# Kernel optimization log

Measured on AMD Instinct MI355X. Metric: run time of the kernel, lower is better.

Reference implementation:

```python
import jax, jax.numpy as jnp
import numpy as np

V, C, T, H, HS, HID, L = 8000, 256, 256, 4, 64, 1024, 2
B = 2


def _ln(x, g, b, eps=1e-5):
    mu = jnp.mean(x, axis=-1, keepdims=True)
    var = jnp.var(x, axis=-1, keepdims=True)
    return (x - mu) * jax.lax.rsqrt(var + eps) * g + b


def setup_inputs() -> dict:
    key = jax.random.key(0)
    ks = iter(jax.random.split(key, 32))
    n = lambda shape: jax.random.normal(next(ks), shape, dtype=jnp.float32) * 0.02
    inp = {
        "idx": jax.random.randint(next(ks), (B, T), 0, V),
        "tok_emb": n((V, C)),
        # distance positional embedding params
        "pos_table": n((T, C)),
        "pos_w1": n((C, 2 * C)),
        "pos_w2": n((2 * C, 2 * C)),
        "pos_b2": n((2 * C,)),
        "pos_ln_g": jnp.ones((2 * C,), jnp.float32),
        "pos_ln_b": jnp.zeros((2 * C,), jnp.float32),
        # per-layer, per-head attention-MLP params (stacked over L, H)
        "att_w1": n((L, H, 2 * C, C)),
        "att_w2": n((L, H, C)),
        "att_b2": n((L, H)),
        "val_w": n((L, H, C, HS)),
        "proj_w": n((L, C, C)),
        "proj_b": n((L, C)),
        "ln2_g": jnp.ones((L, C), jnp.float32),
        "ln2_b": jnp.zeros((L, C), jnp.float32),
        "ff_w1": n((L, C, HID)),
        "ff_w2": n((L, HID, C)),
        "ff_b2": n((L, C)),
        "lnf_g": jnp.ones((C,), jnp.float32),
        "lnf_b": jnp.zeros((C,), jnp.float32),
        "head_w": n((C, V)),
        "head_b": n((V,)),
    }
    return inp


def reference(idx, tok_emb, pos_table, pos_w1, pos_w2, pos_b2, pos_ln_g, pos_ln_b,
              att_w1, att_w2, att_b2, val_w, proj_w, proj_b, ln2_g, ln2_b,
              ff_w1, ff_w2, ff_b2, lnf_g, lnf_b, head_w, head_b):
    b, t = idx.shape
    gelu = lambda x: jax.nn.gelu(x, approximate=False)

    # distance positional embedding: tril(i - j) indices into table
    ar = jnp.arange(t)
    dist = jnp.tril(ar[:, None] - ar[None, :])            # [t,t] in [0, t)
    pe = pos_table[dist]                                   # [t,t,C]
    pe = gelu(pe @ pos_w1) @ pos_w2 + pos_b2               # [t,t,2C]
    pe = _ln(pe, pos_ln_g, pos_ln_b)                       # [t,t,2C]

    mask = jnp.tril(jnp.ones((t, t), bool))                # causal
    scale = C ** (-0.5)

    x = tok_emb[idx]                                       # [b,t,C]
    for l in range(L):
        # pairwise concat(key, query) + pos emb, shared across heads
        kk = jnp.broadcast_to(x[:, None, :, :], (b, t, t, C))   # k[b,i,j]=x[b,j]
        qq = jnp.broadcast_to(x[:, :, None, :], (b, t, t, C))   # q[b,i,j]=x[b,i]
        a2 = jnp.concatenate([kk, qq], axis=-1) + pe[None]       # [b,t,t,2C]
        h1 = gelu(jnp.einsum('btsz,hzc->bhtsc', a2, att_w1[l]))  # [b,H,t,t,C]
        wei = jnp.einsum('bhtsc,hc->bhts', h1, att_w2[l]) + att_b2[l][None, :, None, None]
        wei = wei * scale
        wei = jnp.where(mask[None, None], wei, -jnp.inf)
        wei = jax.nn.softmax(wei, axis=-1)                       # [b,H,t,t]
        v = jnp.einsum('btc,hcd->bhtd', x, val_w[l])             # [b,H,t,HS]
        out = jnp.einsum('bhts,bhsd->bhtd', wei, v)              # [b,H,t,HS]
        out = out.transpose(0, 2, 1, 3).reshape(b, t, H * HS)    # concat heads
        x = x + out @ proj_w[l] + proj_b[l]
        h = _ln(x, ln2_g[l], ln2_b[l])
        x = x + gelu(h @ ff_w1[l]) @ ff_w2[l] + ff_b2[l]
    x = _ln(x, lnf_g, lnf_b)
    logits = x @ head_w + head_b                                 # [b,t,V]
    return logits
```

## Files before the change

### kernel.cpp

```cpp
#include <hip/hip_runtime.h>
#include <hip/hip_bf16.h>
#include <math.h>

constexpr int TDIM = 256;
constexpr int CDIM = 256;
constexpr int NH   = 4;
constexpr int DHS  = 64;
constexpr int FHID = 1024;
constexpr int NV   = 8000;
constexpr int NB   = 2;

typedef __attribute__((ext_vector_type(8))) short bf16x8;
typedef __attribute__((ext_vector_type(4))) float f32x4;
typedef __attribute__((ext_vector_type(2))) float f32x2;
typedef __attribute__((ext_vector_type(4))) unsigned int uint4v;

__device__ __forceinline__ float gelu_f(float x) {
    return 0.5f * x * (1.0f + erff(x * 0.70710678118654752440f));
}

__device__ __forceinline__ f32x2 gelu2(f32x2 x) {
    constexpr float kA = 2.0f * 1.4426950408889634f * 0.7978845608028654f;
    constexpr float kB = kA * 0.044715f;
    f32x2 arg = x * (kA + kB * (x * x));
    arg.x = fminf(arg.x, 120.f);
    arg.y = fminf(arg.y, 120.f);
    float e0 = exp2f(arg.x), e1 = exp2f(arg.y);
    f32x2 num; num.x = x.x * e0; num.y = x.y * e1;
    f32x2 den; den.x = __builtin_amdgcn_rcpf(e0 + 1.f); den.y = __builtin_amdgcn_rcpf(e1 + 1.f);
    return num * den;
}

__device__ __forceinline__ unsigned short f2bf(float f) {
    unsigned int u = __float_as_uint(f);
    unsigned int r = (u + 0x7FFF + ((u >> 16) & 1)) >> 16;
    return (unsigned short)r;
}

__global__ __launch_bounds__(256) void k_tcast_all(
    const float* __restrict__ head_w, const float* __restrict__ att_w1,
    const float* __restrict__ ff_w1, const float* __restrict__ ff_w2,
    const float* __restrict__ val_w, const float* __restrict__ proj_w,
    unsigned short* __restrict__ wT, unsigned short* __restrict__ W1r,
    unsigned short* __restrict__ Wff1, unsigned short* __restrict__ Wff2,
    unsigned short* __restrict__ Wv, unsigned short* __restrict__ Wproj)
{
    int q = blockIdx.x;
    const float* src; unsigned short* dst; int R, C, tx, ty;
    if (q < 2000)      { src = head_w; dst = wT; R = 256; C = 8000; tx = q % 250; ty = q / 250; }
    else if (q < 3024) { int u = q - 2000, s = u >> 7, v = u & 127;
        src = att_w1 + (size_t)s * 512 * 256; dst = W1r + (size_t)s * 512 * 256;
        R = 512; C = 256; tx = v & 7; ty = v >> 3; }
    else if (q < 3536) { int u = q - 3024, s = u >> 8, v = u & 255;
        src = ff_w1 + (size_t)s * 256 * 1024; dst = Wff1 + (size_t)s * 256 * 1024;
        R = 256; C = 1024; tx = v & 31; ty = v >> 5; }
    else if (q < 4048) { int u = q - 3536, s = u >> 8, v = u & 255;
        src = ff_w2 + (size_t)s * 1024 * 256; dst = Wff2 + (size_t)s * 1024 * 256;
        R = 1024; C = 256; tx = v & 7; ty = v >> 3; }
    else if (q < 4176) { int u = q - 4048, s = u >> 4, v = u & 15;
        src = val_w + (size_t)s * 256 * 64; dst = Wv + (size_t)s * 256 * 64;
        R = 256; C = 64; tx = v & 1; ty = v >> 1; }
    else { int u = q - 4176, s = u >> 6, v = u & 63;
        src = proj_w + (size_t)s * 256 * 256; dst = Wproj + (size_t)s * 256 * 256;
        R = 256; C = 256; tx = v & 7; ty = v >> 3; }
    __shared__ float tile[32][33];
    int c0 = tx * 32, r0 = ty * 32, t = threadIdx.x;
    #pragma unroll
    for (int e = 0; e < 4; ++e) {
        int lin = e * 256 + t; int rr = lin >> 5, cc = lin & 31;
        tile[rr][cc] = src[(size_t)(r0 + rr) * C + c0 + cc];
    }
    __syncthreads();
    #pragma unroll
    for (int e = 0; e < 4; ++e) {
        int lin = e * 256 + t; int cc = lin >> 5, rr = lin & 31;
        dst[(size_t)(c0 + cc) * R + r0 + rr] = f2bf(tile[rr][cc]);
    }
}

__global__ void k_embed(const int* __restrict__ idx, const float* __restrict__ tok_emb,
                        float* __restrict__ x, unsigned short* __restrict__ x_bf) {
    int bt = blockIdx.x;
    int c  = threadIdx.x;
    int tok = idx[bt];
    float v = tok_emb[(size_t)tok * CDIM + c];
    x[bt * CDIM + c] = v;
    x_bf[bt * CDIM + c] = f2bf(v);
}

__global__ void k_pe(const float* __restrict__ pos_table, const float* __restrict__ pos_w1,
                     const float* __restrict__ pos_w2, const float* __restrict__ pos_b2,
                     const float* __restrict__ g, const float* __restrict__ bb,
                     unsigned short* __restrict__ ped_bf) {
    int d = blockIdx.x;
    int t = threadIdx.x;
    __shared__ float xs[CDIM];
    __shared__ float hs[512];
    __shared__ float red[512];
    if (t < CDIM) xs[t] = pos_table[d * CDIM + t];
    __syncthreads();
    float acc = 0.f;
    for (int c = 0; c < CDIM; ++c) acc += xs[c] * pos_w1[(size_t)c * 512 + t];
    hs[t] = gelu_f(acc);
    __syncthreads();
    float acc2 = pos_b2[t];
    for (int z = 0; z < 512; ++z) acc2 += hs[z] * pos_w2[(size_t)z * 512 + t];
    red[t] = acc2; __syncthreads();
    for (int s = 256; s > 0; s >>= 1) { if (t < s) red[t] += red[t + s]; __syncthreads(); }
    float mean = red[0] * (1.f / 512.f); __syncthreads();
    float dv = acc2 - mean;
    red[t] = dv * dv; __syncthreads();
    for (int s = 256; s > 0; s >>= 1) { if (t < s) red[t] += red[t + s]; __syncthreads(); }
    float r = rsqrtf(red[0] * (1.f / 512.f) + 1e-5f);
    ped_bf[d * 512 + t] = f2bf(dv * r * g[t] + bb[t]);
}

__device__ __forceinline__ void gemm64_core(
    const unsigned short* __restrict__ A, int lda,
    const unsigned short* __restrict__ B, int ldb,
    int kLen, int t, f32x4 acc[2][2],
    unsigned short* __restrict__ A_lds, unsigned short* __restrict__ B_lds)
{
    int lane = t & 63;
    int w = t >> 6;
    int wm = (w >> 1) * 32, wn = (w & 1) * 32;
    int l15 = lane & 15;
    int lk = (lane >> 4) * 8;
    for (int kc = 0; kc < kLen; kc += 256) {
        #pragma unroll
        for (int it = 0; it < 8; ++it) {
            int chunk = it * 256 + t;
            int row = chunk >> 5;
            int c16 = chunk & 31;
            uint4v va = *(const uint4v*)(A + (size_t)row * lda + kc + c16 * 8);
            uint4v vb = *(const uint4v*)(B + (size_t)row * ldb + kc + c16 * 8);
            int lin = row * 512 + c16 * 16;
            int phys = lin ^ ((row & 7) << 4);
            *(uint4v*)((char*)A_lds + phys) = va;
            *(uint4v*)((char*)B_lds + phys) = vb;
        }
        __syncthreads();
        #pragma unroll
        for (int ks = 0; ks < 8; ++ks) {
            int kb = ks * 32 + lk;
            bf16x8 a[2], b[2];
            #pragma unroll
            for (int f = 0; f < 2; ++f) {
                int mrow = wm + f * 16 + l15;
                int lina = mrow * 512 + kb * 2;
                a[f] = *(const bf16x8*)((const char*)A_lds + (lina ^ ((mrow & 7) << 4)));
                int nrow = wn + f * 16 + l15;
                int linb = nrow * 512 + kb * 2;
                b[f] = *(const bf16x8*)((const char*)B_lds + (linb ^ ((nrow & 7) << 4)));
            }
            acc[0][0] = __builtin_amdgcn_mfma_f32_16x16x32_bf16(a[0], b[0], acc[0][0], 0, 0, 0);
            acc[0][1] = __builtin_amdgcn_mfma_f32_16x16x32_bf16(a[0], b[1], acc[0][1], 0, 0, 0);
            acc[1][0] = __builtin_amdgcn_mfma_f32_16x16x32_bf16(a[1], b[0], acc[1][0], 0, 0, 0);
            acc[1][1] = __builtin_amdgcn_mfma_f32_16x16x32_bf16(a[1], b[1], acc[1][1], 0, 0, 0);
        }
        __syncthreads();
    }
}

__global__ __launch_bounds__(256) void k_qkv(
    const unsigned short* __restrict__ x_bf,
    const unsigned short* __restrict__ ped_bf,
    const unsigned short* __restrict__ W1r,
    const unsigned short* __restrict__ Wv,
    float* __restrict__ PT, float* __restrict__ Qb, float* __restrict__ RT,
    unsigned short* __restrict__ vT_bf, int l)
{
    __shared__ unsigned short A_lds[64 * 256];
    __shared__ unsigned short B_lds[64 * 256];
    int t = threadIdx.x;
    int bid = blockIdx.x;
    int lane = t & 63, w = t >> 6;
    int wm = (w >> 1) * 32, wn = (w & 1) * 32;
    int l15 = lane & 15;
    f32x4 acc[2][2] = {};
    if (bid < 256) {
        int r0 = (bid & 7) * 64;
        int n0 = (bid >> 3) * 64;
        int h = n0 >> 9, isQ = (n0 >> 8) & 1;
        const unsigned short* Bp = W1r + (size_t)l * 1024 * 512
                                 + (size_t)(h * 256 + (n0 & 255)) * 512 + isQ * 256;
        gemm64_core(x_bf + (size_t)r0 * 256, 256, Bp, 512, 256, t, acc, A_lds, B_lds);
        #pragma unroll
        for (int fm = 0; fm < 2; ++fm)
        #pragma unroll
        for (int fn = 0; fn < 2; ++fn) {
            int col = n0 + wn + fn * 16 + l15;
            int c = col & 255;
            #pragma unroll
            for (int r = 0; r < 4; ++r) {
                int row = r0 + wm + fm * 16 + (lane >> 4) * 4 + r;
                int b = row >> 8, ij = row & 255;
                if (isQ) Qb[((b * TDIM + ij) * NH + h) * CDIM + c] = acc[fm][fn][r];
                else     PT[((size_t)(b * NH + h) * CDIM + c) * TDIM + ij] = acc[fm][fn][r];
            }
        }
    } else if (bid < 320) {
        int u = bid - 256;
        int r0 = (u & 3) * 64;
        int n0 = (u >> 2) * 64;
        const unsigned short* Bp = W1r + (size_t)l * 1024 * 512 + (size_t)n0 * 512;
        gemm64_core(ped_bf + (size_t)r0 * 512, 512, Bp, 512, 512, t, acc, A_lds, B_lds);
        #pragma unroll
        for (int fm = 0; fm < 2; ++fm)
        #pragma unroll
        for (int fn = 0; fn < 2; ++fn) {
            int col = n0 + wn + fn * 16 + l15;
            #pragma unroll
            for (int r = 0; r < 4; ++r) {
                int d = r0 + wm + fm * 16 + (lane >> 4) * 4 + r;
                RT[(size_t)col * TDIM + d] = acc[fm][fn][r];
            }
        }
    } else {
        int u = bid - 320;
        int r0 = (u & 7) * 64;
        int n0 = (u >> 3) * 64;
        int h = n0 >> 6;
        const unsigned short* Bp = Wv + ((size_t)l * NH + h) * DHS * CDIM;
        gemm64_core(x_bf + (size_t)r0 * 256, 256, Bp, 256, 256, t, acc, A_lds, B_lds);
        #pragma unroll
        for (int fm = 0; fm < 2; ++fm)
        #pragma unroll
        for (int fn = 0; fn < 2; ++fn) {
            int col = n0 + wn + fn * 16 + l15;
            int d = col & 63;
            #pragma unroll
            for (int r = 0; r < 4; ++r) {
                int row = r0 + wm + fm * 16 + (lane >> 4) * 4 + r;
                int b = row >> 8, j = row & 255;
                vT_bf[(((size_t)b * NH + h) * DHS + d) * TDIM + j] = f2bf(acc[fm][fn][r]);
            }
        }
    }
}

__global__ __launch_bounds__(1024, 8) void k_wei(
    const float* __restrict__ PT, const float* __restrict__ Qb,
    const float* __restrict__ RT, const float* __restrict__ att_w2,
    const float* __restrict__ att_b2, int l, unsigned short* __restrict__ wei_bf) {
    int bid = blockIdx.x;
    int bh = bid & 7;
    int b = bh >> 2, h = bh & 3;
    int i0 = (63 - (bid >> 3)) * 4;
    int t = threadIdx.x;
    int j = t & 255;
    int cs = t >> 8;
    __shared__ float shQW[256][8];
    __shared__ float part[4][4][256];
    { int ii = t >> 8, c = t & 255;
      shQW[c][ii] = Qb[((b * TDIM + (i0 + ii)) * NH + h) * CDIM + c]; }
    if (t < 256) shQW[t][4] = att_w2[(l * NH + h) * CDIM + t];
    __syncthreads();
    f32x2 accA = {0.f, 0.f}, accB = {0.f, 0.f};
    int m = i0 - j;
    int mm = max(m, -3);
    if ((t & 192) <= i0 + 3) {
        const float* pp = PT + ((size_t)(b * NH + h) * CDIM) * TDIM + j;
        const float* rr = RT + ((size_t)h * CDIM) * TDIM + mm;
        int c0 = cs * 64;
        #pragma unroll 4
        for (int c = c0; c < c0 + 64; ++c) {
            float p = pp[(size_t)c * TDIM];
            f32x4 r4; __builtin_memcpy(&r4, rr + (size_t)c * TDIM, 16);
            f32x4 q4 = *(const f32x4*)(&shQW[c][0]);
            float w2v = shQW[c][4];
            f32x2 zA, zB;
            zA.x = p + q4.x + r4.x; zA.y = p + q4.y + r4.y;
            zB.x = p + q4.z + r4.z; zB.y = p + q4.w + r4.w;
            accA += gelu2(zA) * w2v;
            accB += gelu2(zB) * w2v;
        }
    }
    part[cs][0][j] = accA.x; part[cs][1][j] = accA.y;
    part[cs][2][j] = accB.x; part[cs][3][j] = accB.y;
    __syncthreads();
    if (t < 256) {
        #pragma unroll
        for (int ii = 0; ii < 4; ++ii) {
            float s = part[0][ii][t] + part[1][ii][t] + part[2][ii][t] + part[3][ii][t];
            part[0][ii][t] = s;
        }
    }
    __syncthreads();
    if (t < 256) {
        float b2 = att_b2[l * NH + h];
        int lane = t & 63, w = t >> 6;
        int i = i0 + w;
        float lv[4];
        #pragma unroll
        for (int s = 0; s < 4; ++s) {
            int jj = lane + s * 64;
            lv[s] = (jj <= i) ? (part[0][w][jj] + b2) * 0.0625f : -1e30f;
        }
        float mx = fmaxf(fmaxf(lv[0], lv[1]), fmaxf(lv[2], lv[3]));
        #pragma unroll
        for (int off = 32; off; off >>= 1) mx = fmaxf(mx, __shfl_xor(mx, off));
        float es[4], sum = 0.f;
        #pragma unroll
        for (int s = 0; s < 4; ++s) { es[s] = exp2f((lv[s] - mx) * 1.4426950409f); sum += es[s]; }
        #pragma unroll
        for (int off = 32; off; off >>= 1) sum += __shfl_xor(sum, off);
        float inv = 1.0f / sum;
        unsigned short* wrow = wei_bf + (((size_t)bh * TDIM) + i) * TDIM;
        #pragma unroll
        for (int s = 0; s < 4; ++s) wrow[lane + s * 64] = f2bf(es[s] * inv);
    }
}

__global__ __launch_bounds__(256) void k_av_gemm(
    const unsigned short* __restrict__ wei_bf,
    const unsigned short* __restrict__ vT_bf,
    unsigned short* __restrict__ attn_bf)
{
    __shared__ unsigned short A_lds[64 * 256];
    __shared__ unsigned short B_lds[64 * 256];
    int t = threadIdx.x;
    int bid = blockIdx.x;
    int bh = bid >> 2;
    int r0 = (bid & 3) * 64;
    int b = bh >> 2, h = bh & 3;
    f32x4 acc[2][2] = {};
    gemm64_core(wei_bf + (size_t)bh * 65536 + (size_t)r0 * 256, 256,
                vT_bf + (size_t)bh * 16384, 256, 256, t, acc, A_lds, B_lds);
    int lane = t & 63, w = t >> 6;
    int wm = (w >> 1) * 32, wn = (w & 1) * 32;
    int l15 = lane & 15;
    #pragma unroll
    for (int fm = 0; fm < 2; ++fm)
    #pragma unroll
    for (int fn = 0; fn < 2; ++fn) {
        int d = wn + fn * 16 + l15;
        #pragma unroll
        for (int r = 0; r < 4; ++r) {
            int i = r0 + wm + fm * 16 + (lane >> 4) * 4 + r;
            attn_bf[((size_t)(b * TDIM + i)) * CDIM + h * DHS + d] = f2bf(acc[fm][fn][r]);
        }
    }
}

__global__ __launch_bounds__(256) void k_proj_gemm(
    const unsigned short* __restrict__ attn_bf,
    const unsigned short* __restrict__ Wproj,
    const float* __restrict__ proj_b,
    float* __restrict__ pbuf, int l)
{
    __shared__ unsigned short A_lds[64 * 256];
    __shared__ unsigned short B_lds[64 * 256];
    int t = threadIdx.x;
    int r0 = (blockIdx.x & 7) * 64;
    int n0 = (blockIdx.x >> 3) * 64;
    f32x4 acc[2][2] = {};
    gemm64_core(attn_bf + (size_t)r0 * 256, 256,
                Wproj + (size_t)l * 65536 + (size_t)n0 * 256, 256, 256, t, acc, A_lds, B_lds);
    int lane = t & 63, w = t >> 6;
    int wm = (w >> 1) * 32, wn = (w & 1) * 32;
    int l15 = lane & 15;
    #pragma unroll
    for (int fm = 0; fm < 2; ++fm)
    #pragma unroll
    for (int fn = 0; fn < 2; ++fn) {
        int col = n0 + wn + fn * 16 + l15;
        float bb = proj_b[l * CDIM + col];
        #pragma unroll
        for (int r = 0; r < 4; ++r) {
            int row = r0 + wm + fm * 16 + (lane >> 4) * 4 + r;
            pbuf[(size_t)row * CDIM + col] = acc[fm][fn][r] + bb;
        }
    }
}

__global__ void k_resln(const float* __restrict__ pbuf, float* __restrict__ x,
                        const float* __restrict__ lg, const float* __restrict__ lb,
                        unsigned short* __restrict__ hbuf_bf) {
    int bi = blockIdx.x;
    int t = threadIdx.x;
    __shared__ float red[CDIM];
    float val = x[bi * CDIM + t] + pbuf[bi * CDIM + t];
    x[bi * CDIM + t] = val;
    red[t] = val; __syncthreads();
    for (int s = 128; s > 0; s >>= 1) { if (t < s) red[t] += red[t + s]; __syncthreads(); }
    float mean = red[0] * (1.f / 256.f); __syncthreads();
    float dv = val - mean;
    red[t] = dv * dv; __syncthreads();
    for (int s = 128; s > 0; s >>= 1) { if (t < s) red[t] += red[t + s]; __syncthreads(); }
    float r = rsqrtf(red[0] * (1.f / 256.f) + 1e-5f);
    hbuf_bf[bi * CDIM + t] = f2bf(dv * r * lg[t] + lb[t]);
}

__global__ __launch_bounds__(256) void k_ff1_gemm(
    const unsigned short* __restrict__ hbuf_bf,
    const unsigned short* __restrict__ Wff1,
    unsigned short* __restrict__ fbuf_bf, int l)
{
    __shared__ unsigned short A_lds[64 * 256];
    __shared__ unsigned short B_lds[64 * 256];
    int t = threadIdx.x;
    int r0 = blockIdx.x * 64;
    int n0 = blockIdx.y * 64;
    const unsigned short* Bp = Wff1 + (size_t)l * 1024 * 256 + (size_t)n0 * 256;
    f32x4 acc[2][2] = {};
    gemm64_core(hbuf_bf + (size_t)r0 * 256, 256, Bp, 256, 256, t, acc, A_lds, B_lds);
    int lane = t & 63, w = t >> 6;
    int wm = (w >> 1) * 32, wn = (w & 1) * 32;
    int l15 = lane & 15;
    #pragma unroll
    for (int fm = 0; fm < 2; ++fm)
    #pragma unroll
    for (int fn = 0; fn < 2; ++fn) {
        int col = n0 + wn + fn * 16 + l15;
        #pragma unroll
        for (int r = 0; r < 4; ++r) {
            int row = r0 + wm + fm * 16 + (lane >> 4) * 4 + r;
            fbuf_bf[(size_t)row * FHID + col] = f2bf(gelu_f(acc[fm][fn][r]));
        }
    }
}

__global__ __launch_bounds__(256) void k_ff2_gemm(
    const unsigned short* __restrict__ fbuf_bf,
    const unsigned short* __restrict__ Wff2,
    const float* __restrict__ ff_b2,
    float* __restrict__ x, unsigned short* __restrict__ x_bf, int l)
{
    __shared__ unsigned short A_lds[64 * 256];
    __shared__ unsigned short B_lds[64 * 256];
    int t = threadIdx.x;
    int r0 = blockIdx.x * 64;
    int n0 = blockIdx.y * 64;
    const unsigned short* Bp = Wff2 + (size_t)l * 256 * 1024 + (size_t)n0 * 1024;
    f32x4 acc[2][2] = {};
    gemm64_core(fbuf_bf + (size_t)r0 * 1024, 1024, Bp, 1024, 1024, t, acc, A_lds, B_lds);
    int lane = t & 63, w = t >> 6;
    int wm = (w >> 1) * 32, wn = (w & 1) * 32;
    int l15 = lane & 15;
    #pragma unroll
    for (int fm = 0; fm < 2; ++fm)
    #pragma unroll
    for (int fn = 0; fn < 2; ++fn) {
        int col = n0 + wn + fn * 16 + l15;
        float bb = ff_b2[l * CDIM + col];
        #pragma unroll
        for (int r = 0; r < 4; ++r) {
            int row = r0 + wm + fm * 16 + (lane >> 4) * 4 + r;
            float v = x[(size_t)row * CDIM + col] + acc[fm][fn][r] + bb;
            x[(size_t)row * CDIM + col] = v;
            x_bf[(size_t)row * CDIM + col] = f2bf(v);
        }
    }
}

__global__ void k_lnf_bf16(const float* __restrict__ x, const float* __restrict__ g,
                           const float* __restrict__ bb, unsigned short* __restrict__ out) {
    int bi = blockIdx.x;
    int t = threadIdx.x;
    __shared__ float red[CDIM];
    float val = x[bi * CDIM + t];
    red[t] = val; __syncthreads();
    for (int s = 128; s > 0; s >>= 1) { if (t < s) red[t] += red[t + s]; __syncthreads(); }
    float mean = red[0] * (1.f / 256.f); __syncthreads();
    float dv = val - mean;
    red[t] = dv * dv; __syncthreads();
    for (int s = 128; s > 0; s >>= 1) { if (t < s) red[t] += red[t + s]; __syncthreads(); }
    float r = rsqrtf(red[0] * (1.f / 256.f) + 1e-5f);
    out[bi * CDIM + t] = f2bf(dv * r * g[t] + bb[t]);
}

__global__ __launch_bounds__(256) void k_head_mfma(
    const unsigned short* __restrict__ xf_bf,
    const unsigned short* __restrict__ wT,
    const float* __restrict__ head_b,
    float* __restrict__ out)
{
    __shared__ unsigned short A_lds[64 * 256];
    __shared__ unsigned short B_lds[64 * 256];
    int t = threadIdx.x;
    int r0 = blockIdx.x * 64;
    int n0 = blockIdx.y * 64;
    f32x4 acc[2][2] = {};
    gemm64_core(xf_bf + (size_t)r0 * 256, 256, wT + (size_t)n0 * 256, 256, 256,
                t, acc, A_lds, B_lds);
    int lane = t & 63, w = t >> 6;
    int wm = (w >> 1) * 32, wn = (w & 1) * 32;
    int l15 = lane & 15;
    #pragma unroll
    for (int fm = 0; fm < 2; ++fm)
    #pragma unroll
    for (int fn = 0; fn < 2; ++fn) {
        int col = n0 + wn + fn * 16 + l15;
        float hb = head_b[col];
        #pragma unroll
        for (int r = 0; r < 4; ++r) {
            int row = r0 + wm + fm * 16 + (lane >> 4) * 4 + r;
            out[(size_t)row * NV + col] = acc[fm][fn][r] + hb;
        }
    }
}

extern "C" void kernel_launch(void* const* d_in, const int* in_sizes, int n_in,
                              void* d_out, int out_size, void* d_ws, size_t ws_size,
                              hipStream_t stream) {
    const int*   idx       = (const int*)  d_in[0];
    const float* tok_emb   = (const float*)d_in[1];
    const float* pos_table = (const float*)d_in[2];
    const float* pos_w1    = (const float*)d_in[3];
    const float* pos_w2    = (const float*)d_in[4];
    const float* pos_b2    = (const float*)d_in[5];
    const float* pos_ln_g  = (const float*)d_in[6];
    const float* pos_ln_b  = (const float*)d_in[7];
    const float* att_w1    = (const float*)d_in[8];
    const float* att_w2    = (const float*)d_in[9];
    const float* att_b2    = (const float*)d_in[10];
    const float* val_w     = (const float*)d_in[11];
    const float* proj_w    = (const float*)d_in[12];
    const float* proj_b    = (const float*)d_in[13];
    const float* ln2_g     = (const float*)d_in[14];
    const float* ln2_b     = (const float*)d_in[15];
    const float* ff_w1     = (const float*)d_in[16];
    const float* ff_w2     = (const float*)d_in[17];
    const float* ff_b2     = (const float*)d_in[18];
    const float* lnf_g     = (const float*)d_in[19];
    const float* lnf_b     = (const float*)d_in[20];
    const float* head_w    = (const float*)d_in[21];
    const float* head_b    = (const float*)d_in[22];
    float* out = (float*)d_out;

    float* ws = (float*)d_ws;
    float* x    = ws;  ws += NB * TDIM * CDIM;
    float* PT   = ws;  ws += NB * NH * CDIM * TDIM;
    float* Qb   = ws;  ws += NB * TDIM * NH * CDIM;
    ws += 16;
    float* RT   = ws;  ws += NH * CDIM * TDIM;
    float* pbuf = PT;
    unsigned short* x_bf    = (unsigned short*)ws; ws += NB * TDIM * CDIM / 2;
    unsigned short* ped_bf  = (unsigned short*)ws; ws += TDIM * 2 * CDIM / 2;
    unsigned short* hbuf_bf = (unsigned short*)ws; ws += NB * TDIM * CDIM / 2;
    unsigned short* xf_bf   = (unsigned short*)ws; ws += NB * TDIM * CDIM / 2;
    unsigned short* wei_bf  = (unsigned short*)ws; ws += NB * NH * TDIM * TDIM / 2;
    unsigned short* vT_bf   = (unsigned short*)ws; ws += NB * NH * DHS * TDIM / 2;
    unsigned short* attn_bf = (unsigned short*)ws; ws += NB * TDIM * CDIM / 2;
    unsigned short* wT      = (unsigned short*)ws; ws += NV * CDIM / 2;
    unsigned short* W1r     = (unsigned short*)ws; ws += 2 * 1024 * 512 / 2;
    unsigned short* Wff1    = (unsigned short*)ws; ws += 2 * 1024 * 256 / 2;
    unsigned short* Wff2    = (unsigned short*)ws; ws += 2 * 256 * 1024 / 2;
    unsigned short* Wv      = (unsigned short*)ws; ws += 2 * NH * DHS * CDIM / 2;
    unsigned short* Wproj   = (unsigned short*)ws; ws += 2 * CDIM * CDIM / 2;
    unsigned short* fbuf_bf = wei_bf;

    k_tcast_all<<<4304, 256, 0, stream>>>(head_w, att_w1, ff_w1, ff_w2, val_w, proj_w,
                                          wT, W1r, Wff1, Wff2, Wv, Wproj);
    k_embed<<<NB * TDIM, CDIM, 0, stream>>>(idx, tok_emb, x, x_bf);
    k_pe<<<TDIM, 512, 0, stream>>>(pos_table, pos_w1, pos_w2, pos_b2, pos_ln_g, pos_ln_b, ped_bf);

    for (int l = 0; l < 2; ++l) {
        k_qkv<<<352, 256, 0, stream>>>(x_bf, ped_bf, W1r, Wv, PT, Qb, RT, vT_bf, l);
        k_wei<<<NB * NH * TDIM / 4, 1024, 0, stream>>>(PT, Qb, RT, att_w2, att_b2, l, wei_bf);
        k_av_gemm<<<32, 256, 0, stream>>>(wei_bf, vT_bf, attn_bf);
        k_proj_gemm<<<32, 256, 0, stream>>>(attn_bf, Wproj, proj_b, pbuf, l);
        k_resln<<<NB * TDIM, 256, 0, stream>>>(pbuf, x, ln2_g + l * CDIM, ln2_b + l * CDIM, hbuf_bf);
        k_ff1_gemm<<<dim3(8, 16), 256, 0, stream>>>(hbuf_bf, Wff1, fbuf_bf, l);
        k_ff2_gemm<<<dim3(8, 4), 256, 0, stream>>>(fbuf_bf, Wff2, ff_b2, x, x_bf, l);
    }

    k_lnf_bf16<<<NB * TDIM, 256, 0, stream>>>(x, lnf_g, lnf_b, xf_bf);
    k_head_mfma<<<dim3(8, 125), 256, 0, stream>>>(xf_bf, wT, head_b, out);
}
```

Measured before the change: 344.2 us.

## Fuse attention-value product into softmax kernel and merge embedding with positional prologue

```diff
diff --git a/kernel.cpp b/kernel.cpp
--- a/kernel.cpp
+++ b/kernel.cpp
@@ -78,22 +78,26 @@
     }
 }
 
-__global__ void k_embed(const int* __restrict__ idx, const float* __restrict__ tok_emb,
-                        float* __restrict__ x, unsigned short* __restrict__ x_bf) {
-    int bt = blockIdx.x;
-    int c  = threadIdx.x;
-    int tok = idx[bt];
-    float v = tok_emb[(size_t)tok * CDIM + c];
-    x[bt * CDIM + c] = v;
-    x_bf[bt * CDIM + c] = f2bf(v);
-}
-
-__global__ void k_pe(const float* __restrict__ pos_table, const float* __restrict__ pos_w1,
-                     const float* __restrict__ pos_w2, const float* __restrict__ pos_b2,
-                     const float* __restrict__ g, const float* __restrict__ bb,
-                     unsigned short* __restrict__ ped_bf) {
-    int d = blockIdx.x;
-    int t = threadIdx.x;
+__global__ __launch_bounds__(512) void k_pre(
+    const int* __restrict__ idx, const float* __restrict__ tok_emb,
+    const float* __restrict__ pos_table, const float* __restrict__ pos_w1,
+    const float* __restrict__ pos_w2, const float* __restrict__ pos_b2,
+    const float* __restrict__ g, const float* __restrict__ bb,
+    float* __restrict__ x, unsigned short* __restrict__ x_bf,
+    unsigned short* __restrict__ ped_bf)
+{
+    int bid = blockIdx.x;
+    int t = threadIdx.x;
+    if (bid < 256) {
+        int r = bid * 2 + (t >> 8);
+        int c = t & 255;
+        int tok = idx[r];
+        float v = tok_emb[(size_t)tok * CDIM + c];
+        x[r * CDIM + c] = v;
+        x_bf[r * CDIM + c] = f2bf(v);
+        return;
+    }
+    int d = bid - 256;
     __shared__ float xs[CDIM];
     __shared__ float hs[512];
     __shared__ float red[512];
@@ -126,31 +130,31 @@
     int wm = (w >> 1) * 32, wn = (w & 1) * 32;
     int l15 = lane & 15;
     int lk = (lane >> 4) * 8;
-    for (int kc = 0; kc < kLen; kc += 256) {
-        #pragma unroll
-        for (int it = 0; it < 8; ++it) {
+    for (int kc = 0; kc < kLen; kc += 128) {
+        #pragma unroll
+        for (int it = 0; it < 4; ++it) {
             int chunk = it * 256 + t;
-            int row = chunk >> 5;
-            int c16 = chunk & 31;
+            int row = chunk >> 4;
+            int c16 = chunk & 15;
             uint4v va = *(const uint4v*)(A + (size_t)row * lda + kc + c16 * 8);
             uint4v vb = *(const uint4v*)(B + (size_t)row * ldb + kc + c16 * 8);
-            int lin = row * 512 + c16 * 16;
+            int lin = row * 256 + c16 * 16;
             int phys = lin ^ ((row & 7) << 4);
             *(uint4v*)((char*)A_lds + phys) = va;
             *(uint4v*)((char*)B_lds + phys) = vb;
         }
         __syncthreads();
         #pragma unroll
-        for (int ks = 0; ks < 8; ++ks) {
+        for (int ks = 0; ks < 4; ++ks) {
             int kb = ks * 32 + lk;
             bf16x8 a[2], b[2];
             #pragma unroll
             for (int f = 0; f < 2; ++f) {
                 int mrow = wm + f * 16 + l15;
-                int lina = mrow * 512 + kb * 2;
+                int lina = mrow * 256 + kb * 2;
                 a[f] = *(const bf16x8*)((const char*)A_lds + (lina ^ ((mrow & 7) << 4)));
                 int nrow = wn + f * 16 + l15;
-                int linb = nrow * 512 + kb * 2;
+                int linb = nrow * 256 + kb * 2;
                 b[f] = *(const bf16x8*)((const char*)B_lds + (linb ^ ((nrow & 7) << 4)));
             }
             acc[0][0] = __builtin_amdgcn_mfma_f32_16x16x32_bf16(a[0], b[0], acc[0][0], 0, 0, 0);
@@ -168,10 +172,10 @@
     const unsigned short* __restrict__ W1r,
     const unsigned short* __restrict__ Wv,
     float* __restrict__ PT, float* __restrict__ Qb, float* __restrict__ RT,
-    unsigned short* __restrict__ vT_bf, int l)
-{
-    __shared__ unsigned short A_lds[64 * 256];
-    __shared__ unsigned short B_lds[64 * 256];
+    float* __restrict__ vbuf, int l)
+{
+    __shared__ unsigned short A_lds[64 * 128];
+    __shared__ unsigned short B_lds[64 * 128];
     int t = threadIdx.x;
     int bid = blockIdx.x;
     int lane = t & 63, w = t >> 6;
@@ -233,7 +237,7 @@
             for (int r = 0; r < 4; ++r) {
                 int row = r0 + wm + fm * 16 + (lane >> 4) * 4 + r;
                 int b = row >> 8, j = row & 255;
-                vT_bf[(((size_t)b * NH + h) * DHS + d) * TDIM + j] = f2bf(acc[fm][fn][r]);
+                vbuf[((size_t)(b * NH + h) * TDIM + j) * DHS + d] = acc[fm][fn][r];
             }
         }
     }
@@ -242,7 +246,8 @@
 __global__ __launch_bounds__(1024, 8) void k_wei(
     const float* __restrict__ PT, const float* __restrict__ Qb,
     const float* __restrict__ RT, const float* __restrict__ att_w2,
-    const float* __restrict__ att_b2, int l, unsigned short* __restrict__ wei_bf) {
+    const float* __restrict__ att_b2, const float* __restrict__ vbuf,
+    int l, unsigned short* __restrict__ attn_bf) {
     int bid = blockIdx.x;
     int bh = bid & 7;
     int b = bh >> 2, h = bh & 3;
@@ -252,6 +257,8 @@
     int cs = t >> 8;
     __shared__ float shQW[256][8];
     __shared__ float part[4][4][256];
+    __shared__ float p_lds[4][256];
+    __shared__ float pvp[4][4][64];
     { int ii = t >> 8, c = t & 255;
       shQW[c][ii] = Qb[((b * TDIM + (i0 + ii)) * NH + h) * CDIM + c]; }
     if (t < 256) shQW[t][4] = att_w2[(l * NH + h) * CDIM + t];
@@ -260,18 +267,21 @@
     int m = i0 - j;
     int mm = max(m, -3);
     if ((t & 192) <= i0 + 3) {
-        const float* pp = PT + ((size_t)(b * NH + h) * CDIM) * TDIM + j;
-        const float* rr = RT + ((size_t)h * CDIM) * TDIM + mm;
-        int c0 = cs * 64;
+        const float* pk = PT + ((size_t)(b * NH + h) * CDIM + cs * 64) * TDIM + j;
+        const float* rk = RT + ((size_t)h * CDIM + cs * 64) * TDIM + mm;
+        float p_n = *pk;
+        f32x4 r_n; __builtin_memcpy(&r_n, rk, 16);
         #pragma unroll 4
-        for (int c = c0; c < c0 + 64; ++c) {
-            float p = pp[(size_t)c * TDIM];
-            f32x4 r4; __builtin_memcpy(&r4, rr + (size_t)c * TDIM, 16);
+        for (int k = 0; k < 64; ++k) {
+            float p_c = p_n; f32x4 r_c = r_n;
+            pk += TDIM; rk += TDIM;
+            if (k < 63) { p_n = *pk; __builtin_memcpy(&r_n, rk, 16); }
+            int c = cs * 64 + k;
             f32x4 q4 = *(const f32x4*)(&shQW[c][0]);
             float w2v = shQW[c][4];
             f32x2 zA, zB;
-            zA.x = p + q4.x + r4.x; zA.y = p + q4.y + r4.y;
-            zB.x = p + q4.z + r4.z; zB.y = p + q4.w + r4.w;
+            zA.x = p_c + q4.x + r_c.x; zA.y = p_c + q4.y + r_c.y;
+            zB.x = p_c + q4.z + r_c.z; zB.y = p_c + q4.w + r_c.w;
             accA += gelu2(zA) * w2v;
             accB += gelu2(zB) * w2v;
         }
@@ -306,40 +316,25 @@
         #pragma unroll
         for (int off = 32; off; off >>= 1) sum += __shfl_xor(sum, off);
         float inv = 1.0f / sum;
-        unsigned short* wrow = wei_bf + (((size_t)bh * TDIM) + i) * TDIM;
-        #pragma unroll
-        for (int s = 0; s < 4; ++s) wrow[lane + s * 64] = f2bf(es[s] * inv);
-    }
-}
-
-__global__ __launch_bounds__(256) void k_av_gemm(
-    const unsigned short* __restrict__ wei_bf,
-    const unsigned short* __restrict__ vT_bf,
-    unsigned short* __restrict__ attn_bf)
-{
-    __shared__ unsigned short A_lds[64 * 256];
-    __shared__ unsigned short B_lds[64 * 256];
-    int t = threadIdx.x;
-    int bid = blockIdx.x;
-    int bh = bid >> 2;
-    int r0 = (bid & 3) * 64;
-    int b = bh >> 2, h = bh & 3;
-    f32x4 acc[2][2] = {};
-    gemm64_core(wei_bf + (size_t)bh * 65536 + (size_t)r0 * 256, 256,
-                vT_bf + (size_t)bh * 16384, 256, 256, t, acc, A_lds, B_lds);
-    int lane = t & 63, w = t >> 6;
-    int wm = (w >> 1) * 32, wn = (w & 1) * 32;
-    int l15 = lane & 15;
-    #pragma unroll
-    for (int fm = 0; fm < 2; ++fm)
-    #pragma unroll
-    for (int fn = 0; fn < 2; ++fn) {
-        int d = wn + fn * 16 + l15;
-        #pragma unroll
-        for (int r = 0; r < 4; ++r) {
-            int i = r0 + wm + fm * 16 + (lane >> 4) * 4 + r;
-            attn_bf[((size_t)(b * TDIM + i)) * CDIM + h * DHS + d] = f2bf(acc[fm][fn][r]);
-        }
+        #pragma unroll
+        for (int s = 0; s < 4; ++s) p_lds[w][lane + s * 64] = es[s] * inv;
+    }
+    __syncthreads();
+    {
+        int strip = t >> 8, row = (t >> 6) & 3, d = t & 63;
+        const float* vp = vbuf + ((size_t)(b * NH + h) * TDIM + strip * 64) * DHS + d;
+        const float* pl = &p_lds[row][strip * 64];
+        float acc = 0.f;
+        #pragma unroll 8
+        for (int jj = 0; jj < 64; ++jj)
+            acc = fmaf(pl[jj], vp[(size_t)jj * DHS], acc);
+        pvp[strip][row][d] = acc;
+    }
+    __syncthreads();
+    if (t < 256) {
+        int row = t >> 6, d = t & 63;
+        float s = pvp[0][row][d] + pvp[1][row][d] + pvp[2][row][d] + pvp[3][row][d];
+        attn_bf[((size_t)(b * TDIM + i0 + row)) * CDIM + h * DHS + d] = f2bf(s);
     }
 }
 
@@ -349,8 +344,8 @@
     const float* __restrict__ proj_b,
     float* __restrict__ pbuf, int l)
 {
-    __shared__ unsigned short A_lds[64 * 256];
-    __shared__ unsigned short B_lds[64 * 256];
+    __shared__ unsigned short A_lds[64 * 128];
+    __shared__ unsigned short B_lds[64 * 128];
     int t = threadIdx.x;
     int r0 = (blockIdx.x & 7) * 64;
     int n0 = (blockIdx.x >> 3) * 64;
@@ -397,8 +392,8 @@
     const unsigned short* __restrict__ Wff1,
     unsigned short* __restrict__ fbuf_bf, int l)
 {
-    __shared__ unsigned short A_lds[64 * 256];
-    __shared__ unsigned short B_lds[64 * 256];
+    __shared__ unsigned short A_lds[64 * 128];
+    __shared__ unsigned short B_lds[64 * 128];
     int t = threadIdx.x;
     int r0 = blockIdx.x * 64;
     int n0 = blockIdx.y * 64;
@@ -427,8 +422,8 @@
     const float* __restrict__ ff_b2,
     float* __restrict__ x, unsigned short* __restrict__ x_bf, int l)
 {
-    __shared__ unsigned short A_lds[64 * 256];
-    __shared__ unsigned short B_lds[64 * 256];
+    __shared__ unsigned short A_lds[64 * 128];
+    __shared__ unsigned short B_lds[64 * 128];
     int t = threadIdx.x;
     int r0 = blockIdx.x * 64;
     int n0 = blockIdx.y * 64;
@@ -476,8 +471,8 @@
     const float* __restrict__ head_b,
     float* __restrict__ out)
 {
-    __shared__ unsigned short A_lds[64 * 256];
-    __shared__ unsigned short B_lds[64 * 256];
+    __shared__ unsigned short A_lds[64 * 128];
+    __shared__ unsigned short B_lds[64 * 128];
     int t = threadIdx.x;
     int r0 = blockIdx.x * 64;
     int n0 = blockIdx.y * 64;
@@ -535,31 +530,30 @@
     float* Qb   = ws;  ws += NB * TDIM * NH * CDIM;
     ws += 16;
     float* RT   = ws;  ws += NH * CDIM * TDIM;
+    float* vbuf = ws;  ws += NB * NH * TDIM * DHS;
     float* pbuf = PT;
     unsigned short* x_bf    = (unsigned short*)ws; ws += NB * TDIM * CDIM / 2;
     unsigned short* ped_bf  = (unsigned short*)ws; ws += TDIM * 2 * CDIM / 2;
     unsigned short* hbuf_bf = (unsigned short*)ws; ws += NB * TDIM * CDIM / 2;
     unsigned short* xf_bf   = (unsigned short*)ws; ws += NB * TDIM * CDIM / 2;
-    unsigned short* wei_bf  = (unsigned short*)ws; ws += NB * NH * TDIM * TDIM / 2;
-    unsigned short* vT_bf   = (unsigned short*)ws; ws += NB * NH * DHS * TDIM / 2;
     unsigned short* attn_bf = (unsigned short*)ws; ws += NB * TDIM * CDIM / 2;
+    unsigned short* fbuf_bf = (unsigned short*)ws; ws += NB * TDIM * FHID / 2;
     unsigned short* wT      = (unsigned short*)ws; ws += NV * CDIM / 2;
     unsigned short* W1r     = (unsigned short*)ws; ws += 2 * 1024 * 512 / 2;
     unsigned short* Wff1    = (unsigned short*)ws; ws += 2 * 1024 * 256 / 2;
     unsigned short* Wff2    = (unsigned short*)ws; ws += 2 * 256 * 1024 / 2;
     unsigned short* Wv      = (unsigned short*)ws; ws += 2 * NH * DHS * CDIM / 2;
     unsigned short* Wproj   = (unsigned short*)ws; ws += 2 * CDIM * CDIM / 2;
-    unsigned short* fbuf_bf = wei_bf;
 
     k_tcast_all<<<4304, 256, 0, stream>>>(head_w, att_w1, ff_w1, ff_w2, val_w, proj_w,
                                           wT, W1r, Wff1, Wff2, Wv, Wproj);
-    k_embed<<<NB * TDIM, CDIM, 0, stream>>>(idx, tok_emb, x, x_bf);
-    k_pe<<<TDIM, 512, 0, stream>>>(pos_table, pos_w1, pos_w2, pos_b2, pos_ln_g, pos_ln_b, ped_bf);
+    k_pre<<<512, 512, 0, stream>>>(idx, tok_emb, pos_table, pos_w1, pos_w2, pos_b2,
+                                   pos_ln_g, pos_ln_b, x, x_bf, ped_bf);
 
     for (int l = 0; l < 2; ++l) {
-        k_qkv<<<352, 256, 0, stream>>>(x_bf, ped_bf, W1r, Wv, PT, Qb, RT, vT_bf, l);
-        k_wei<<<NB * NH * TDIM / 4, 1024, 0, stream>>>(PT, Qb, RT, att_w2, att_b2, l, wei_bf);
-        k_av_gemm<<<32, 256, 0, stream>>>(wei_bf, vT_bf, attn_bf);
+        k_qkv<<<352, 256, 0, stream>>>(x_bf, ped_bf, W1r, Wv, PT, Qb, RT, vbuf, l);
+        k_wei<<<NB * NH * TDIM / 4, 1024, 0, stream>>>(PT, Qb, RT, att_w2, att_b2, vbuf,
+                                                       l, attn_bf);
         k_proj_gemm<<<32, 256, 0, stream>>>(attn_bf, Wproj, proj_b, pbuf, l);
         k_resln<<<NB * TDIM, 256, 0, stream>>>(pbuf, x, ln2_g + l * CDIM, ln2_b + l * CDIM, hbuf_bf);
         k_ff1_gemm<<<dim3(8, 16), 256, 0, stream>>>(hbuf_bf, Wff1, fbuf_bf, l);
```

Measured after the change: 352.4 us. 2.4% more time.
